# Optimization experiments

Measured on AMD Instinct MI355X. Metric: run time of the kernel, lower is better.

The kernel has to match this reference:

```python
import jax, jax.numpy as jnp
import numpy as np

N = 65536       # num nodes
F = 128         # num_features
D = 256         # embedding_dim
E = N * 8       # num edges
CS = 32         # target_cluster_size
DEPTH = 8
H = 8
NCLS = 10


def setup_inputs() -> dict:
    key = jax.random.key(0)
    ks = jax.random.split(key, 16)
    r = lambda k, shp: (jax.random.normal(k, shp, jnp.float32) * 0.02)
    return {
        "x": jax.random.normal(ks[0], (N, F), jnp.float32),
        "edge_index": jax.random.randint(ks[1], (2, E), 0, N),
        "W_in": r(ks[2], (F, D)), "b_in": jnp.zeros((D,), jnp.float32),
        "W_gat": r(ks[3], (D, D)), "a_src": r(ks[4], (D,)), "a_dst": r(ks[5], (D,)),
        "b_gat": jnp.zeros((D,), jnp.float32),
        "W_emb": r(ks[6], (CS * D, D)), "b_emb": jnp.zeros((D,), jnp.float32),
        "class_tok": r(ks[7], (D,)),
        "ln1_s": jnp.ones((DEPTH, D), jnp.float32), "ln1_b": jnp.zeros((DEPTH, D), jnp.float32),
        "Wqkv": r(ks[8], (DEPTH, D, 3 * D)), "bqkv": jnp.zeros((DEPTH, 3 * D), jnp.float32),
        "Wproj": r(ks[9], (DEPTH, D, D)), "bproj": jnp.zeros((DEPTH, D), jnp.float32),
        "ln2_s": jnp.ones((DEPTH, D), jnp.float32), "ln2_b": jnp.zeros((DEPTH, D), jnp.float32),
        "W1": r(ks[10], (DEPTH, D, 4 * D)), "b1": jnp.zeros((DEPTH, 4 * D), jnp.float32),
        "W2": r(ks[11], (DEPTH, 4 * D, D)), "b2": jnp.zeros((DEPTH, D), jnp.float32),
        "W_cls": r(ks[12], (D, NCLS)), "b_cls": jnp.zeros((NCLS,), jnp.float32),
    }


def _layernorm(x, s, b):
    m = jnp.mean(x, -1, keepdims=True)
    v = jnp.var(x, -1, keepdims=True)
    return (x - m) * jax.lax.rsqrt(v + 1e-5) * s + b


def _forward(x, edge_index, W_in, b_in, W_gat, a_src, a_dst, b_gat, W_emb, b_emb,
             class_tok, ln1_s, ln1_b, Wqkv, bqkv, Wproj, bproj, ln2_s, ln2_b,
             W1, b1, W2, b2, W_cls, b_cls):
    # input_layer: LazyLinear(F -> D)
    h = x @ W_in + b_in                                   # [N, D]
    # GATConv(D -> D), 1 head, add_self_loops=True
    loop = jnp.arange(N)
    src = jnp.concatenate([edge_index[0], loop])          # message source j
    dst = jnp.concatenate([edge_index[1], loop])          # message target i
    Wh = h @ W_gat                                        # [N, D]
    e = jax.nn.leaky_relu((Wh @ a_src)[src] + (Wh @ a_dst)[dst], 0.2)
    emax = jax.ops.segment_max(e, dst, num_segments=N)
    ee = jnp.exp(e - emax[dst])
    denom = jax.ops.segment_sum(ee, dst, num_segments=N)
    alpha = ee / denom[dst]                               # softmax over incoming edges
    h = jax.ops.segment_sum(alpha[:, None] * Wh[src], dst, num_segments=N) + b_gat
    # clusters of 32 contiguous nodes: gather, flatten, embeddings_layer (32*D -> D)
    tok = h.reshape(N // CS, CS * D) @ W_emb + b_emb      # [num_clusters, D]
    seq = jnp.concatenate([class_tok[None, :], tok])[None]  # [1, S, D], S = num_clusters + 1
    scale = (D // H) ** -0.5
    for i in range(DEPTH):
        y = _layernorm(seq, ln1_s[i], ln1_b[i])
        qkv = (y @ Wqkv[i] + bqkv[i]).reshape(1, -1, 3, H, D // H)
        q, k, v = qkv[:, :, 0], qkv[:, :, 1], qkv[:, :, 2]
        att = jax.nn.softmax(jnp.einsum('bshd,bthd->bhst', q, k) * scale, axis=-1)
        o = jnp.einsum('bhst,bthd->bshd', att, v).reshape(1, -1, D)
        seq = seq + (o @ Wproj[i] + bproj[i])
        y = _layernorm(seq, ln2_s[i], ln2_b[i])
        seq = seq + (jax.nn.gelu(y @ W1[i] + b1[i], approximate=False) @ W2[i] + b2[i])
    # to_class on the class token
    return seq[0, 0][None, :] @ W_cls + b_cls             # [1, NCLS]


def reference(x, edge_index, W_in, b_in, W_gat, a_src, a_dst, b_gat, W_emb, b_emb,
              class_tok, ln1_s, ln1_b, Wqkv, bqkv, Wproj, bproj, ln2_s, ln2_b,
              W1, b1, W2, b2, W_cls, b_cls):
    return _forward(x, edge_index, W_in, b_in, W_gat, a_src, a_dst, b_gat, W_emb,
                    b_emb, class_tok, ln1_s, ln1_b, Wqkv, bqkv, Wproj, bproj,
                    ln2_s, ln2_b, W1, b1, W2, b2, W_cls, b_cls)
```

## Files before the change

### kernel.cpp

```cpp
#include <hip/hip_runtime.h>
#include <math.h>

#define N_NODES 65536
#define F_IN 128
#define D_MODEL 256
#define E_EDGES 524288
#define EE_EDGES 589824
#define SEQ_LEN 2049
#define SEQ_PAD 2112
#define NHEAD 8
#define HDIM 32
#define NCLS 10
#define NSPLIT 4

typedef unsigned short u16;
typedef __attribute__((ext_vector_type(8))) short s8v;
typedef __attribute__((ext_vector_type(4))) float f4v;

__device__ __forceinline__ u16 f2bf(float f)
{
    union { float f; unsigned u; } v; v.f = f;
    unsigned r = v.u + 0x7FFF + ((v.u >> 16) & 1);
    return (u16)(r >> 16);
}
__device__ __forceinline__ float bf2f(u16 h)
{
    union { unsigned u; float f; } v; v.u = ((unsigned)h) << 16;
    return v.f;
}

__global__ __launch_bounds__(256) void prep_weight(
    const float* __restrict__ W, u16* __restrict__ Oh, u16* __restrict__ Ol,
    int K, int N, long long strideW, long long strideO, int write_lo)
{
    const float* Wz = W + (size_t)blockIdx.z * strideW;
    u16* Ohz = Oh + (size_t)blockIdx.z * strideO;
    u16* Olz = Ol + (size_t)blockIdx.z * strideO;
    __shared__ u16 th[64][68];
    __shared__ u16 tl[64][68];
    int kb = blockIdx.x * 64, nb = blockIdx.y * 64;
    int t = threadIdx.x;
    int kr = t >> 4, nc = (t & 15) * 4;
#pragma unroll
    for (int i = 0; i < 4; ++i) {
        int k = kr + i * 16;
        float4 v = *(const float4*)(Wz + (size_t)(kb + k) * N + nb + nc);
        float vv[4] = {v.x, v.y, v.z, v.w};
#pragma unroll
        for (int e = 0; e < 4; ++e) {
            u16 h = f2bf(vv[e]);
            th[k][nc + e] = h;
            if (write_lo) tl[k][nc + e] = f2bf(vv[e] - bf2f(h));
        }
    }
    __syncthreads();
    int nr = t >> 4, kc = (t & 15) * 4;
#pragma unroll
    for (int i = 0; i < 4; ++i) {
        int n = nr + i * 16;
        uint2 oh;
        oh.x = (unsigned)th[kc + 0][n] | ((unsigned)th[kc + 1][n] << 16);
        oh.y = (unsigned)th[kc + 2][n] | ((unsigned)th[kc + 3][n] << 16);
        *(uint2*)(Ohz + (size_t)(nb + n) * K + kb + kc) = oh;
        if (write_lo) {
            uint2 ol;
            ol.x = (unsigned)tl[kc + 0][n] | ((unsigned)tl[kc + 1][n] << 16);
            ol.y = (unsigned)tl[kc + 2][n] | ((unsigned)tl[kc + 3][n] << 16);
            *(uint2*)(Olz + (size_t)(nb + n) * K + kb + kc) = ol;
        }
    }
}

template<int ACT, int RES, int ATOM, int OB, int APRE, int TERMS>
__global__ __launch_bounds__(256) void hgemm(
    const void* __restrict__ A, const u16* __restrict__ Al2,
    const u16* __restrict__ Bh, const u16* __restrict__ Bl,
    const float* __restrict__ bias, const float* __restrict__ Rsd,
    float* __restrict__ C, u16* __restrict__ C2,
    int M, int N, int K, int Kc)
{
    __shared__ __align__(16) u16 SS[(TERMS == 3 ? 4 : 2) * 2048];
    u16* const AhS = SS;
    u16* const BhS = SS + 2048;
    u16* const AlS = SS + 4096;
    u16* const BlS = SS + 6144;
    const int tid = threadIdx.x;
    const int bn = blockIdx.x * 64, bm = blockIdx.y * 64;
    const int kb = blockIdx.z * Kc;
    const int r = tid >> 2, cch = tid & 3;
    const int widx = r * 32 + ((cch ^ ((r >> 1) & 3)) << 3);
    const int w = tid >> 6, lane = tid & 63;
    const int wm = w >> 1, wn = w & 1;
    const int lr = lane & 15, lc = lane >> 4;
    const int ar0 = wm * 32 + lr, ar1 = ar0 + 16;
    const int nr0 = wn * 32 + lr, nr1 = nr0 + 16;
    const int ai0 = ar0 * 32 + ((lc ^ ((ar0 >> 1) & 3)) << 3);
    const int ai1 = ar1 * 32 + ((lc ^ ((ar1 >> 1) & 3)) << 3);
    const int bi0 = nr0 * 32 + ((lc ^ ((nr0 >> 1) & 3)) << 3);
    const int bi1 = nr1 * 32 + ((lc ^ ((nr1 >> 1) & 3)) << 3);

    f4v acc00 = {0.f, 0.f, 0.f, 0.f}, acc01 = acc00, acc10 = acc00, acc11 = acc00;

    const int gr = bm + r;
    const float* apf = (const float*)A + (size_t)gr * K + kb + cch * 8;
    const u16*   aph = (const u16*)A + (size_t)gr * K + kb + cch * 8;
    const u16*   apl = Al2 ? Al2 + (size_t)gr * K + kb + cch * 8 : (const u16*)0;
    const u16* bhp = Bh + (size_t)(bn + r) * K + kb + cch * 8;
    const u16* blp = (TERMS == 3) ? Bl + (size_t)(bn + r) * K + kb + cch * 8
                                  : (const u16*)0;

    for (int k0 = 0; k0 < Kc; k0 += 32) {
        s8v hv = {0, 0, 0, 0, 0, 0, 0, 0}, lv = hv;
        if (APRE) {
            if (gr < M) {
                hv = *(const s8v*)aph;
                if (TERMS == 3) lv = *(const s8v*)apl;
            }
        } else {
            float v[8] = {0.f, 0.f, 0.f, 0.f, 0.f, 0.f, 0.f, 0.f};
            if (gr < M) {
                float4 x0 = *(const float4*)apf;
                float4 x1 = *(const float4*)(apf + 4);
                v[0] = x0.x; v[1] = x0.y; v[2] = x0.z; v[3] = x0.w;
                v[4] = x1.x; v[5] = x1.y; v[6] = x1.z; v[7] = x1.w;
            }
#pragma unroll
            for (int e = 0; e < 8; ++e) {
                u16 h = f2bf(v[e]);
                hv[e] = (short)h;
                if (TERMS == 3) lv[e] = (short)f2bf(v[e] - bf2f(h));
            }
        }
        *(s8v*)&AhS[widx] = hv;
        *(s8v*)&BhS[widx] = *(const s8v*)bhp;
        if (TERMS == 3) {
            *(s8v*)&AlS[widx] = lv;
            *(s8v*)&BlS[widx] = *(const s8v*)blp;
        }
        __syncthreads();

        s8v a0h = *(s8v*)&AhS[ai0], a1h = *(s8v*)&AhS[ai1];
        s8v b0h = *(s8v*)&BhS[bi0], b1h = *(s8v*)&BhS[bi1];
        acc00 = __builtin_amdgcn_mfma_f32_16x16x32_bf16(a0h, b0h, acc00, 0, 0, 0);
        acc01 = __builtin_amdgcn_mfma_f32_16x16x32_bf16(a0h, b1h, acc01, 0, 0, 0);
        acc10 = __builtin_amdgcn_mfma_f32_16x16x32_bf16(a1h, b0h, acc10, 0, 0, 0);
        acc11 = __builtin_amdgcn_mfma_f32_16x16x32_bf16(a1h, b1h, acc11, 0, 0, 0);
        if (TERMS == 3) {
            s8v a0l = *(s8v*)&AlS[ai0], a1l = *(s8v*)&AlS[ai1];
            s8v b0l = *(s8v*)&BlS[bi0], b1l = *(s8v*)&BlS[bi1];
            acc00 = __builtin_amdgcn_mfma_f32_16x16x32_bf16(a0h, b0l, acc00, 0, 0, 0);
            acc00 = __builtin_amdgcn_mfma_f32_16x16x32_bf16(a0l, b0h, acc00, 0, 0, 0);
            acc01 = __builtin_amdgcn_mfma_f32_16x16x32_bf16(a0h, b1l, acc01, 0, 0, 0);
            acc01 = __builtin_amdgcn_mfma_f32_16x16x32_bf16(a0l, b1h, acc01, 0, 0, 0);
            acc10 = __builtin_amdgcn_mfma_f32_16x16x32_bf16(a1h, b0l, acc10, 0, 0, 0);
            acc10 = __builtin_amdgcn_mfma_f32_16x16x32_bf16(a1l, b0h, acc10, 0, 0, 0);
            acc11 = __builtin_amdgcn_mfma_f32_16x16x32_bf16(a1h, b1l, acc11, 0, 0, 0);
            acc11 = __builtin_amdgcn_mfma_f32_16x16x32_bf16(a1l, b1h, acc11, 0, 0, 0);
        }
        __syncthreads();
        apf += 32; aph += 32; if (TERMS == 3) apl += 32;
        bhp += 32; if (TERMS == 3) blp += 32;
    }

#pragma unroll
    for (int fg = 0; fg < 4; ++fg) {
        int f = fg >> 1, g = fg & 1;
        f4v a = (fg == 0) ? acc00 : (fg == 1) ? acc01 : (fg == 2) ? acc10 : acc11;
        int col = bn + wn * 32 + g * 16 + lr;
        int row0 = bm + wm * 32 + f * 16 + lc * 4;
#pragma unroll
        for (int j = 0; j < 4; ++j) {
            int rr = row0 + j;
            if (rr < M) {
                float vv = a[j];
                if (ATOM) {
                    atomicAdd(&C[(size_t)rr * N + col], vv);
                } else {
                    if (bias) vv += bias[col];
                    if (ACT == 1) vv = 0.5f * vv * (1.0f + erff(vv * 0.70710678118654752f));
                    if (RES) vv += Rsd[(size_t)rr * N + col];
                    if (OB == 1) ((u16*)C)[(size_t)rr * N + col] = f2bf(vv);
                    else         C[(size_t)rr * N + col] = vv;
                }
            }
        }
    }
    (void)C2;
}

__global__ void init_bias(float* __restrict__ C, const float* __restrict__ bias,
                          int total, int nmask)
{
    int i = blockIdx.x * 256 + threadIdx.x;
    if (i < total) C[i] = bias[i & nmask];
}

__global__ void pad_zero_u32(unsigned* __restrict__ p, int n)
{
    int i = blockIdx.x * 256 + threadIdx.x;
    if (i < n) p[i] = 0u;
}

__global__ void vecmat256(const float* __restrict__ v, const float* __restrict__ W,
                          float* __restrict__ out)
{
    int n = threadIdx.x;
    float acc = 0.f;
    for (int k = 0; k < 256; ++k) acc += v[k] * W[k * 256 + n];
    out[n] = acc;
}

__global__ void gat_init(float* __restrict__ emax, float* __restrict__ denom,
                         int* __restrict__ deg)
{
    int i = blockIdx.x * 256 + threadIdx.x;
    emax[i] = -1e30f;
    denom[i] = 0.f;
    deg[i] = 0;
}

__global__ __launch_bounds__(256) void gat_scores(
    const u16* __restrict__ WH, const float* __restrict__ a_src,
    const float* __restrict__ a_dst, float* __restrict__ s_src,
    float* __restrict__ s_dst)
{
    int gid = blockIdx.x * 256 + threadIdx.x;
    int node = gid >> 6;
    int lane = gid & 63;
    uint2 rv = *(const uint2*)(WH + (size_t)node * D_MODEL + (lane << 2));
    float d0 = __uint_as_float(rv.x << 16);
    float d1 = __uint_as_float(rv.x & 0xffff0000u);
    float d2 = __uint_as_float(rv.y << 16);
    float d3 = __uint_as_float(rv.y & 0xffff0000u);
    float4 asv = *(const float4*)(a_src + (lane << 2));
    float4 adv = *(const float4*)(a_dst + (lane << 2));
    float as = d0 * asv.x + d1 * asv.y + d2 * asv.z + d3 * asv.w;
    float ad = d0 * adv.x + d1 * adv.y + d2 * adv.z + d3 * adv.w;
#pragma unroll
    for (int off = 32; off; off >>= 1) {
        as += __shfl_down(as, off);
        ad += __shfl_down(ad, off);
    }
    if (lane == 0) { s_src[node] = as; s_dst[node] = ad; }
}

__device__ __forceinline__ void atomicMaxFloat(float* addr, float val)
{
    int* ai = (int*)addr;
    int old = __float_as_int(*addr);
    while (__int_as_float(old) < val) {
        int prev = atomicCAS(ai, old, __float_as_int(val));
        if (prev == old) break;
        old = prev;
    }
}

__global__ void edge_pass1(const int* __restrict__ ei, const float* __restrict__ s_src,
                           const float* __restrict__ s_dst, float* __restrict__ e_buf,
                           float* __restrict__ emax, int* __restrict__ deg)
{
    int j = blockIdx.x * 256 + threadIdx.x;
    if (j >= EE_EDGES) return;
    int s, d;
    if (j < E_EDGES) { s = ei[j]; d = ei[E_EDGES + j]; }
    else { s = d = j - E_EDGES; }
    float e = s_src[s] + s_dst[d];
    e = (e > 0.f) ? e : 0.2f * e;
    e_buf[j] = e;
    atomicMaxFloat(&emax[d], e);
    atomicAdd(&deg[d], 1);
}

__global__ void scan1(const int* __restrict__ in, int* __restrict__ out_excl,
                      int* __restrict__ bsum)
{
    __shared__ int s[256];
    int t = threadIdx.x;
    int i = blockIdx.x * 256 + t;
    int v = in[i];
    s[t] = v;
    __syncthreads();
    for (int off = 1; off < 256; off <<= 1) {
        int u = (t >= off) ? s[t - off] : 0;
        __syncthreads();
        s[t] += u;
        __syncthreads();
    }
    out_excl[i] = s[t] - v;
    if (t == 255) bsum[blockIdx.x] = s[255];
}

__global__ void scan2(int* __restrict__ bsum)
{
    __shared__ int s[256];
    int t = threadIdx.x;
    int v = bsum[t];
    s[t] = v;
    __syncthreads();
    for (int off = 1; off < 256; off <<= 1) {
        int u = (t >= off) ? s[t - off] : 0;
        __syncthreads();
        s[t] += u;
        __syncthreads();
    }
    bsum[t] = s[t] - v;
}

__global__ void scan3(int* __restrict__ offs, const int* __restrict__ bsum,
                      int* __restrict__ cur)
{
    int i = blockIdx.x * 256 + threadIdx.x;
    int v = offs[i] + bsum[blockIdx.x];
    offs[i] = v;
    cur[i] = v;
}

__global__ void edge_pass2(const int* __restrict__ ei, const float* __restrict__ e_buf,
                           const float* __restrict__ emax, float* __restrict__ denom,
                           int* __restrict__ cur, int* __restrict__ csr_src,
                           float* __restrict__ csr_w)
{
    int j = blockIdx.x * 256 + threadIdx.x;
    if (j >= EE_EDGES) return;
    int s, d;
    if (j < E_EDGES) { s = ei[j]; d = ei[E_EDGES + j]; }
    else { s = d = j - E_EDGES; }
    float ee = __expf(e_buf[j] - emax[d]);
    atomicAdd(&denom[d], ee);
    int pos = atomicAdd(&cur[d], 1);
    csr_src[pos] = s;
    csr_w[pos] = ee;
}

__global__ __launch_bounds__(256) void gat_aggregate(
    const u16* __restrict__ WH, const int* __restrict__ csr_src,
    const float* __restrict__ csr_w, const int* __restrict__ offs,
    const int* __restrict__ deg, const float* __restrict__ denom,
    const float* __restrict__ b_gat, u16* __restrict__ hH)
{
    int gid = blockIdx.x * 256 + threadIdx.x;
    int node = gid >> 6;
    int lane = gid & 63;
    float inv = 1.0f / denom[node];
    float a0 = 0.f, a1 = 0.f, a2 = 0.f, a3 = 0.f;
    int s0 = offs[node], e0 = s0 + deg[node];
    for (int k = s0; k < e0; ++k) {
        int src = csr_src[k];
        float alpha = csr_w[k] * inv;
        uint2 rv = *(const uint2*)(WH + (size_t)src * D_MODEL + (lane << 2));
        a0 += alpha * __uint_as_float(rv.x << 16);
        a1 += alpha * __uint_as_float(rv.x & 0xffff0000u);
        a2 += alpha * __uint_as_float(rv.y << 16);
        a3 += alpha * __uint_as_float(rv.y & 0xffff0000u);
    }
    float4 bg = *(const float4*)(b_gat + (lane << 2));
    float v0 = a0 + bg.x, v1 = a1 + bg.y, v2 = a2 + bg.z, v3 = a3 + bg.w;
    uint2 ho;
    ho.x = (unsigned)f2bf(v0) | ((unsigned)f2bf(v1) << 16);
    ho.y = (unsigned)f2bf(v2) | ((unsigned)f2bf(v3) << 16);
    *(uint2*)(hH + (size_t)node * D_MODEL + (lane << 2)) = ho;
}

__global__ __launch_bounds__(256) void ln_kernel(
    float* __restrict__ seqio, const float* __restrict__ sc,
    const float* __restrict__ bi, u16* __restrict__ Yh,
    const float* __restrict__ badd)
{
    int row = blockIdx.x;
    int t = threadIdx.x;
    float x = seqio[(size_t)row * 256 + t];
    float sum = x, sq = x * x;
#pragma unroll
    for (int off = 32; off; off >>= 1) {
        sum += __shfl_down(sum, off);
        sq  += __shfl_down(sq, off);
    }
    __shared__ float rs[4], rq[4];
    if ((t & 63) == 0) { rs[t >> 6] = sum; rq[t >> 6] = sq; }
    __syncthreads();
    sum = rs[0] + rs[1] + rs[2] + rs[3];
    sq  = rq[0] + rq[1] + rq[2] + rq[3];
    float mean = sum * (1.f / 256.f);
    float var  = sq * (1.f / 256.f) - mean * mean;
    float r = rsqrtf(var + 1e-5f);
    float y = (x - mean) * r * sc[t] + bi[t];
    Yh[(size_t)row * 256 + t] = f2bf(y);
    seqio[(size_t)row * 256 + t] = x + badd[t];
}

__global__ __launch_bounds__(256) void mfma_attn_split(
    const u16* __restrict__ QKV, float* __restrict__ Opart,
    float* __restrict__ Mpart, float* __restrict__ Lpart)
{
    __shared__ __align__(16) u16 Ks[64 * 32];
    __shared__ __align__(16) u16 Vt[32 * 72];
    __shared__ __align__(16) u16 Ps[4 * 16 * 72];
    const int tid = threadIdx.x;
    const int w = tid >> 6, lane = tid & 63;
    const int g = lane >> 4, ql = lane & 15;
    const int h = blockIdx.y;
    const int sp = blockIdx.z;
    const int t0 = (33 * sp) / NSPLIT, t1 = (33 * (sp + 1)) / NSPLIT;
    const int qbase = blockIdx.x * 64 + w * 16;
    const float scale = 0.17677669529663687f;

    int qrow = qbase + ql; if (qrow > SEQ_LEN - 1) qrow = SEQ_LEN - 1;
    const s8v qfrag = *(const s8v*)(QKV + (size_t)qrow * 768 + h * 32 + g * 8);

    f4v o0 = {0.f, 0.f, 0.f, 0.f}, o1 = o0;
    float m[4], l[4];
#pragma unroll
    for (int r = 0; r < 4; ++r) { m[r] = -1e30f; l[r] = 0.f; }

    const int sr = tid >> 2, sc_ = tid & 3;
    const int kslot = sc_ ^ ((sr >> 1) & 3);
    u16* const psw = &Ps[w * 1152];

    for (int t = t0; t < t1; ++t) {
        __syncthreads();
        {
            int grow = t * 64 + sr;
            const u16* kp = QKV + (size_t)grow * 768 + 256 + h * 32 + sc_ * 8;
            s8v kvv = *(const s8v*)kp;
            s8v vvv = *(const s8v*)(kp + 256);
            *(s8v*)&Ks[sr * 32 + kslot * 8] = kvv;
#pragma unroll
            for (int e = 0; e < 8; ++e) Vt[(sc_ * 8 + e) * 72 + sr] = (u16)vvv[e];
        }
        __syncthreads();

        f4v s[4];
        const f4v zz = {0.f, 0.f, 0.f, 0.f};
#pragma unroll
        for (int c = 0; c < 4; ++c) {
            int kvloc = c * 16 + ql;
            s8v kf = *(s8v*)&Ks[kvloc * 32 + ((g ^ ((kvloc >> 1) & 3)) << 3)];
            s[c] = __builtin_amdgcn_mfma_f32_16x16x32_bf16(qfrag, kf, zz, 0, 0, 0);
            int kvg = t * 64 + kvloc;
            bool valid = (kvg < SEQ_LEN);
#pragma unroll
            for (int r = 0; r < 4; ++r)
                s[c][r] = valid ? s[c][r] * scale : -1e30f;
        }

        float mloc[4];
#pragma unroll
        for (int r = 0; r < 4; ++r) {
            float v = fmaxf(fmaxf(s[0][r], s[1][r]), fmaxf(s[2][r], s[3][r]));
            v = fmaxf(v, __shfl_xor(v, 1));
            v = fmaxf(v, __shfl_xor(v, 2));
            v = fmaxf(v, __shfl_xor(v, 4));
            v = fmaxf(v, __shfl_xor(v, 8));
            mloc[r] = v;
        }
        float fac[4];
#pragma unroll
        for (int r = 0; r < 4; ++r) {
            float mn = fmaxf(m[r], mloc[r]);
            fac[r] = __expf(m[r] - mn);
            m[r] = mn;
        }
#pragma unroll
        for (int c = 0; c < 4; ++c)
#pragma unroll
            for (int r = 0; r < 4; ++r)
                s[c][r] = __expf(s[c][r] - m[r]);
#pragma unroll
        for (int r = 0; r < 4; ++r) {
            float ls = s[0][r] + s[1][r] + s[2][r] + s[3][r];
            ls += __shfl_xor(ls, 1);
            ls += __shfl_xor(ls, 2);
            ls += __shfl_xor(ls, 4);
            ls += __shfl_xor(ls, 8);
            l[r] = l[r] * fac[r] + ls;
            o0[r] *= fac[r];
            o1[r] *= fac[r];
        }

#pragma unroll
        for (int c = 0; c < 4; ++c)
#pragma unroll
            for (int r = 0; r < 4; ++r)
                psw[(g * 4 + r) * 72 + c * 16 + ql] = f2bf(s[c][r]);

#pragma unroll
        for (int kch = 0; kch < 2; ++kch) {
            s8v pf = *(s8v*)&psw[ql * 72 + kch * 32 + g * 8];
            s8v v0 = *(s8v*)&Vt[ql * 72 + kch * 32 + g * 8];
            s8v v1 = *(s8v*)&Vt[(16 + ql) * 72 + kch * 32 + g * 8];
            o0 = __builtin_amdgcn_mfma_f32_16x16x32_bf16(pf, v0, o0, 0, 0, 0);
            o1 = __builtin_amdgcn_mfma_f32_16x16x32_bf16(pf, v1, o1, 0, 0, 0);
        }
    }

#pragma unroll
    for (int r = 0; r < 4; ++r) {
        int q = qbase + g * 4 + r;
        if (q < SEQ_LEN) {
            size_t base = ((size_t)sp * SEQ_PAD + q) * 256 + h * 32;
            Opart[base + ql] = o0[r];
            Opart[base + 16 + ql] = o1[r];
            if (ql == 0) {
                Mpart[((size_t)sp * SEQ_PAD + q) * NHEAD + h] = m[r];
                Lpart[((size_t)sp * SEQ_PAD + q) * NHEAD + h] = l[r];
            }
        }
    }
}

__global__ __launch_bounds__(256) void attn_combine(
    const float* __restrict__ Opart, const float* __restrict__ Mpart,
    const float* __restrict__ Lpart, u16* __restrict__ Oh)
{
    int q = blockIdx.x;
    int t = threadIdx.x;
    int h = t >> 5, d = t & 31;
    float ms[NSPLIT], ls[NSPLIT];
    float M = -1e30f;
#pragma unroll
    for (int s = 0; s < NSPLIT; ++s) {
        ms[s] = Mpart[((size_t)s * SEQ_PAD + q) * NHEAD + h];
        ls[s] = Lpart[((size_t)s * SEQ_PAD + q) * NHEAD + h];
        M = fmaxf(M, ms[s]);
    }
    float L = 0.f, O = 0.f;
#pragma unroll
    for (int s = 0; s < NSPLIT; ++s) {
        float f = __expf(ms[s] - M);
        L += ls[s] * f;
        O += Opart[((size_t)s * SEQ_PAD + q) * 256 + h * 32 + d] * f;
    }
    Oh[(size_t)q * 256 + h * 32 + d] = f2bf(O / L);
}

__global__ void seed_seq(const float* __restrict__ cls, float* __restrict__ seq)
{
    seq[threadIdx.x] = cls[threadIdx.x];
}

__global__ void cls_head(const float* __restrict__ seq, const float* __restrict__ W,
                         const float* __restrict__ b, float* __restrict__ out)
{
    __shared__ float s[256];
    int t = threadIdx.x;
    s[t] = seq[t];
    __syncthreads();
    if (t < NCLS) {
        float acc = b[t];
        for (int k = 0; k < 256; ++k) acc += s[k] * W[k * NCLS + t];
        out[t] = acc;
    }
}

extern "C" void kernel_launch(void* const* d_in, const int* in_sizes, int n_in,
                              void* d_out, int out_size, void* d_ws, size_t ws_size,
                              hipStream_t stream)
{
    (void)in_sizes; (void)n_in; (void)out_size; (void)ws_size;
    const float* x       = (const float*)d_in[0];
    const int*   ei      = (const int*)d_in[1];
    const float* W_in    = (const float*)d_in[2];
    const float* b_in    = (const float*)d_in[3];
    const float* W_gat   = (const float*)d_in[4];
    const float* a_src   = (const float*)d_in[5];
    const float* a_dst   = (const float*)d_in[6];
    const float* b_gat   = (const float*)d_in[7];
    const float* W_emb   = (const float*)d_in[8];
    const float* b_emb   = (const float*)d_in[9];
    const float* cls_tok = (const float*)d_in[10];
    const float* ln1_s   = (const float*)d_in[11];
    const float* ln1_b   = (const float*)d_in[12];
    const float* Wqkv    = (const float*)d_in[13];
    const float* bqkv    = (const float*)d_in[14];
    const float* Wproj   = (const float*)d_in[15];
    const float* bproj   = (const float*)d_in[16];
    const float* ln2_s   = (const float*)d_in[17];
    const float* ln2_b   = (const float*)d_in[18];
    const float* W1      = (const float*)d_in[19];
    const float* b1      = (const float*)d_in[20];
    const float* W2      = (const float*)d_in[21];
    const float* b2      = (const float*)d_in[22];
    const float* W_cls   = (const float*)d_in[23];
    const float* b_cls   = (const float*)d_in[24];
    float* out = (float*)d_out;

    float* ws = (float*)d_ws;
    u16*   bufWHu = (u16*)ws;
    float* seqb  = ws;
    u16*   Yh    = (u16*)(ws + 524544);
    u16*   QKVb  = (u16*)(ws + 1049088);
    u16*   Oh    = (u16*)(ws + 1860096);
    u16*   MLPHh = (u16*)(ws + 2384640);
    u16*   wreg  = (u16*)(ws + 5500000);
    u16* embh  = wreg;
    u16* embl  = wreg + 2097152;
    u16* qkvh  = wreg + 4194304;
    u16* qkvl  = wreg + 5767168;
    u16* projh = wreg + 7340032;
    u16* projl = wreg + 7864320;
    u16* w1h   = wreg + 8388608;
    u16* w1l   = wreg + 10485760;
    u16* w2h   = wreg + 12582912;
    u16* w2l   = wreg + 14680064;
    u16*   hH    = (u16*)(ws + 16777216);
    float* Opart = ws + 16777216;
    float* Mpart = Opart + (size_t)NSPLIT * SEQ_PAD * 256;
    float* Lpart = Mpart + (size_t)NSPLIT * SEQ_PAD * NHEAD;
    float* sm    = ws + 2 * 16777216;
    float* s_src = sm;
    float* s_dst = sm + 65536;
    float* emaxb = sm + 2 * 65536;
    float* denom = sm + 3 * 65536;
    float* e_buf = sm + 4 * 65536;
    float* csr_w = e_buf + 589824;
    float* Wc    = csr_w + 589824;
    float* bc    = Wc + 32768;
    int*   deg     = (int*)(bc + 256);
    int*   offs    = deg + 65536;
    int*   cur     = offs + 65536;
    int*   bsum    = cur + 65536;
    int*   csr_src = bsum + 256;
    u16*   wgTh = (u16*)(csr_src + 589824);
    u16*   wgTl = wgTh + 65536;
    u16*   wcTh = wgTh + 131072;
    u16*   wcTl = wcTh + 32768;

    gat_init<<<256, 256, 0, stream>>>(emaxb, denom, deg);
    prep_weight<<<dim3(4, 4, 1), 256, 0, stream>>>(W_gat, wgTh, wgTl, 256, 256, 0, 0, 1);
    hgemm<0,0,0,0,0,3><<<dim3(4, 2, 1), 256, 0, stream>>>(
        W_in, nullptr, wgTh, wgTl, nullptr, nullptr, Wc, nullptr, 128, 256, 256, 256);
    vecmat256<<<1, 256, 0, stream>>>(b_in, W_gat, bc);
    prep_weight<<<dim3(2, 4, 1), 256, 0, stream>>>(Wc, wcTh, wcTl, 128, 256, 0, 0, 0);
    hgemm<0,0,0,1,0,1><<<dim3(4, 1024, 1), 256, 0, stream>>>(
        x, nullptr, wcTh, nullptr, bc, nullptr, (float*)bufWHu, nullptr,
        N_NODES, 256, 128, 128);
    gat_scores<<<16384, 256, 0, stream>>>(bufWHu, a_src, a_dst, s_src, s_dst);
    edge_pass1<<<EE_EDGES / 256, 256, 0, stream>>>(ei, s_src, s_dst, e_buf, emaxb, deg);
    scan1<<<256, 256, 0, stream>>>(deg, offs, bsum);
    scan2<<<1, 256, 0, stream>>>(bsum);
    scan3<<<256, 256, 0, stream>>>(offs, bsum, cur);
    edge_pass2<<<EE_EDGES / 256, 256, 0, stream>>>(ei, e_buf, emaxb, denom, cur,
                                                   csr_src, csr_w);
    gat_aggregate<<<16384, 256, 0, stream>>>(bufWHu, csr_src, csr_w, offs, deg,
                                             denom, b_gat, hH);

    prep_weight<<<dim3(128, 4, 1), 256, 0, stream>>>(W_emb, embh, embl, 8192, 256, 0, 0, 0);
    prep_weight<<<dim3(4, 12, 8), 256, 0, stream>>>(Wqkv, qkvh, qkvl, 256, 768,
                                                    196608, 196608, 0);
    prep_weight<<<dim3(4, 4, 8), 256, 0, stream>>>(Wproj, projh, projl, 256, 256,
                                                   65536, 65536, 0);
    prep_weight<<<dim3(4, 16, 8), 256, 0, stream>>>(W1, w1h, w1l, 256, 1024,
                                                    262144, 262144, 0);
    prep_weight<<<dim3(16, 4, 8), 256, 0, stream>>>(W2, w2h, w2l, 1024, 256,
                                                    262144, 262144, 0);

    init_bias<<<2048, 256, 0, stream>>>(seqb + 256, b_emb, 2048 * 256, 255);
    hgemm<0,0,1,0,1,1><<<dim3(4, 32, 8), 256, 0, stream>>>(
        (const void*)hH, nullptr, embh, nullptr, nullptr, nullptr, seqb + 256,
        nullptr, 2048, 256, 8192, 1024);
    seed_seq<<<1, 256, 0, stream>>>(cls_tok, seqb);

    pad_zero_u32<<<95, 256, 0, stream>>>(
        (unsigned*)(QKVb + (size_t)SEQ_LEN * 768), (SEQ_PAD - SEQ_LEN) * 768 / 2);

    for (int i = 0; i < 8; ++i) {
        ln_kernel<<<SEQ_LEN, 256, 0, stream>>>(seqb, ln1_s + i * 256,
                                               ln1_b + i * 256, Yh,
                                               bproj + i * 256);
        hgemm<0,0,0,1,1,1><<<dim3(12, 33, 1), 256, 0, stream>>>(
            (const void*)Yh, nullptr, qkvh + (size_t)i * 196608, nullptr,
            bqkv + i * 768, nullptr, (float*)QKVb, nullptr, SEQ_LEN, 768, 256, 256);
        mfma_attn_split<<<dim3(33, NHEAD, NSPLIT), 256, 0, stream>>>(
            QKVb, Opart, Mpart, Lpart);
        attn_combine<<<SEQ_LEN, 256, 0, stream>>>(Opart, Mpart, Lpart, Oh);
        hgemm<0,0,1,0,1,1><<<dim3(4, 33, 4), 256, 0, stream>>>(
            (const void*)Oh, nullptr, projh + (size_t)i * 65536, nullptr,
            nullptr, nullptr, seqb, nullptr, SEQ_LEN, 256, 256, 64);
        ln_kernel<<<SEQ_LEN, 256, 0, stream>>>(seqb, ln2_s + i * 256,
                                               ln2_b + i * 256, Yh,
                                               b2 + i * 256);
        hgemm<1,0,0,1,1,1><<<dim3(16, 33, 1), 256, 0, stream>>>(
            (const void*)Yh, nullptr, w1h + (size_t)i * 262144, nullptr,
            b1 + i * 1024, nullptr, (float*)MLPHh, nullptr, SEQ_LEN, 1024, 256, 256);
        hgemm<0,0,1,0,1,1><<<dim3(4, 33, 4), 256, 0, stream>>>(
            (const void*)MLPHh, nullptr, w2h + (size_t)i * 262144, nullptr,
            nullptr, nullptr, seqb, nullptr, SEQ_LEN, 256, 1024, 256);
    }

    cls_head<<<1, 256, 0, stream>>>(seqb, W_cls, b_cls, out);
}
```

Before: 1.045 ms.

## Fuse LayerNorm into QKV and MLP-up GEMMs by folding scale/bias into weights

Removes the standalone LayerNorm kernels. The LN scale is folded into the bf16 weights at prep time, and the LN bias is folded into the GEMM bias through a new bias_fold kernel. The QKV and W1 GEMMs now read the fp32 residual stream directly and compute per-row mean and rstd in a prologue before normalizing on the fly. Residual biases (bproj, b2) move into the split-K atomic GEMMs on z==0, and the seq init is merged into one kernel. This cuts launches and the Yh round trip, but each GEMM block re-reads its A rows to compute the statistics, and the variance is computed as E[x^2]-mu^2.

```diff
diff --git a/kernel.cpp b/kernel.cpp
--- a/kernel.cpp
+++ b/kernel.cpp
@@ -31,11 +31,13 @@
 
 __global__ __launch_bounds__(256) void prep_weight(
     const float* __restrict__ W, u16* __restrict__ Oh, u16* __restrict__ Ol,
-    int K, int N, long long strideW, long long strideO, int write_lo)
+    int K, int N, long long strideW, long long strideO, int write_lo,
+    const float* __restrict__ scale)
 {
     const float* Wz = W + (size_t)blockIdx.z * strideW;
     u16* Ohz = Oh + (size_t)blockIdx.z * strideO;
     u16* Olz = Ol + (size_t)blockIdx.z * strideO;
+    const float* scz = scale ? scale + (size_t)blockIdx.z * D_MODEL : nullptr;
     __shared__ u16 th[64][68];
     __shared__ u16 tl[64][68];
     int kb = blockIdx.x * 64, nb = blockIdx.y * 64;
@@ -44,8 +46,9 @@
 #pragma unroll
     for (int i = 0; i < 4; ++i) {
         int k = kr + i * 16;
+        float sv = scz ? scz[kb + k] : 1.f;
         float4 v = *(const float4*)(Wz + (size_t)(kb + k) * N + nb + nc);
-        float vv[4] = {v.x, v.y, v.z, v.w};
+        float vv[4] = {v.x * sv, v.y * sv, v.z * sv, v.w * sv};
 #pragma unroll
         for (int e = 0; e < 4; ++e) {
             u16 h = f2bf(vv[e]);
@@ -71,7 +74,21 @@
     }
 }
 
-template<int ACT, int RES, int ATOM, int OB, int APRE, int TERMS>
+__global__ void bias_fold(const float* __restrict__ lnb, const float* __restrict__ W,
+                          const float* __restrict__ b0, float* __restrict__ out,
+                          int N, long long strideW)
+{
+    int z = blockIdx.y;
+    int n = blockIdx.x * 256 + threadIdx.x;
+    if (n >= N) return;
+    const float* Wz = W + (size_t)z * strideW;
+    const float* lz = lnb + (size_t)z * D_MODEL;
+    float acc = b0[(size_t)z * N + n];
+    for (int k = 0; k < D_MODEL; ++k) acc += lz[k] * Wz[(size_t)k * N + n];
+    out[(size_t)z * N + n] = acc;
+}
+
+template<int ACT, int RES, int ATOM, int OB, int APRE, int TERMS, int LNA>
 __global__ __launch_bounds__(256) void hgemm(
     const void* __restrict__ A, const u16* __restrict__ Al2,
     const u16* __restrict__ Bh, const u16* __restrict__ Bl,
@@ -109,6 +126,28 @@
     const u16* blp = (TERMS == 3) ? Bl + (size_t)(bn + r) * K + kb + cch * 8
                                   : (const u16*)0;
 
+    float mu_r = 0.f, rs_r = 1.f;
+    if (LNA) {
+        float s1 = 0.f, s2 = 0.f;
+        if (gr < M) {
+            const float* rowp = apf;
+            for (int ks = 0; ks < Kc / 32; ++ks) {
+                float4 a0 = *(const float4*)(rowp);
+                float4 a1 = *(const float4*)(rowp + 4);
+                s1 += a0.x + a0.y + a0.z + a0.w + a1.x + a1.y + a1.z + a1.w;
+                s2 += a0.x*a0.x + a0.y*a0.y + a0.z*a0.z + a0.w*a0.w
+                    + a1.x*a1.x + a1.y*a1.y + a1.z*a1.z + a1.w*a1.w;
+                rowp += 32;
+            }
+        }
+        s1 += __shfl_xor(s1, 1); s1 += __shfl_xor(s1, 2);
+        s2 += __shfl_xor(s2, 1); s2 += __shfl_xor(s2, 2);
+        float mu = s1 * (1.f / 256.f);
+        float var = s2 * (1.f / 256.f) - mu * mu;
+        mu_r = mu;
+        rs_r = rsqrtf(var + 1e-5f);
+    }
+
     for (int k0 = 0; k0 < Kc; k0 += 32) {
         s8v hv = {0, 0, 0, 0, 0, 0, 0, 0}, lv = hv;
         if (APRE) {
@@ -126,9 +165,10 @@
             }
 #pragma unroll
             for (int e = 0; e < 8; ++e) {
-                u16 h = f2bf(v[e]);
+                float vv = LNA ? (v[e] - mu_r) * rs_r : v[e];
+                u16 h = f2bf(vv);
                 hv[e] = (short)h;
-                if (TERMS == 3) lv[e] = (short)f2bf(v[e] - bf2f(h));
+                if (TERMS == 3) lv[e] = (short)f2bf(vv - bf2f(h));
             }
         }
         *(s8v*)&AhS[widx] = hv;
@@ -174,6 +214,7 @@
             if (rr < M) {
                 float vv = a[j];
                 if (ATOM) {
+                    if (bias && blockIdx.z == 0) vv += bias[col];
                     atomicAdd(&C[(size_t)rr * N + col], vv);
                 } else {
                     if (bias) vv += bias[col];
@@ -188,11 +229,12 @@
     (void)C2;
 }
 
-__global__ void init_bias(float* __restrict__ C, const float* __restrict__ bias,
-                          int total, int nmask)
-{
-    int i = blockIdx.x * 256 + threadIdx.x;
-    if (i < total) C[i] = bias[i & nmask];
+__global__ void init_seq(float* __restrict__ seq, const float* __restrict__ bias,
+                         const float* __restrict__ cls)
+{
+    int row = blockIdx.x;
+    int t = threadIdx.x;
+    seq[(size_t)row * 256 + t] = (row == 0) ? cls[t] : bias[t];
 }
 
 __global__ void pad_zero_u32(unsigned* __restrict__ p, int n)
@@ -361,33 +403,6 @@
     *(uint2*)(hH + (size_t)node * D_MODEL + (lane << 2)) = ho;
 }
 
-__global__ __launch_bounds__(256) void ln_kernel(
-    float* __restrict__ seqio, const float* __restrict__ sc,
-    const float* __restrict__ bi, u16* __restrict__ Yh,
-    const float* __restrict__ badd)
-{
-    int row = blockIdx.x;
-    int t = threadIdx.x;
-    float x = seqio[(size_t)row * 256 + t];
-    float sum = x, sq = x * x;
-#pragma unroll
-    for (int off = 32; off; off >>= 1) {
-        sum += __shfl_down(sum, off);
-        sq  += __shfl_down(sq, off);
-    }
-    __shared__ float rs[4], rq[4];
-    if ((t & 63) == 0) { rs[t >> 6] = sum; rq[t >> 6] = sq; }
-    __syncthreads();
-    sum = rs[0] + rs[1] + rs[2] + rs[3];
-    sq  = rq[0] + rq[1] + rq[2] + rq[3];
-    float mean = sum * (1.f / 256.f);
-    float var  = sq * (1.f / 256.f) - mean * mean;
-    float r = rsqrtf(var + 1e-5f);
-    float y = (x - mean) * r * sc[t] + bi[t];
-    Yh[(size_t)row * 256 + t] = f2bf(y);
-    seqio[(size_t)row * 256 + t] = x + badd[t];
-}
-
 __global__ __launch_bounds__(256) void mfma_attn_split(
     const u16* __restrict__ QKV, float* __restrict__ Opart,
     float* __restrict__ Mpart, float* __restrict__ Lpart)
@@ -531,11 +546,6 @@
         O += Opart[((size_t)s * SEQ_PAD + q) * 256 + h * 32 + d] * f;
     }
     Oh[(size_t)q * 256 + h * 32 + d] = f2bf(O / L);
-}
-
-__global__ void seed_seq(const float* __restrict__ cls, float* __restrict__ seq)
-{
-    seq[threadIdx.x] = cls[threadIdx.x];
 }
 
 __global__ void cls_head(const float* __restrict__ seq, const float* __restrict__ W,
@@ -587,10 +597,11 @@
     float* ws = (float*)d_ws;
     u16*   bufWHu = (u16*)ws;
     float* seqb  = ws;
-    u16*   Yh    = (u16*)(ws + 524544);
     u16*   QKVb  = (u16*)(ws + 1049088);
     u16*   Oh    = (u16*)(ws + 1860096);
     u16*   MLPHh = (u16*)(ws + 2384640);
+    float* qkvBias = ws + 3500000;
+    float* w1Bias  = qkvBias + 8 * 768;
     u16*   wreg  = (u16*)(ws + 5500000);
     u16* embh  = wreg;
     u16* embl  = wreg + 2097152;
@@ -626,12 +637,14 @@
     u16*   wcTl = wcTh + 32768;
 
     gat_init<<<256, 256, 0, stream>>>(emaxb, denom, deg);
-    prep_weight<<<dim3(4, 4, 1), 256, 0, stream>>>(W_gat, wgTh, wgTl, 256, 256, 0, 0, 1);
-    hgemm<0,0,0,0,0,3><<<dim3(4, 2, 1), 256, 0, stream>>>(
+    prep_weight<<<dim3(4, 4, 1), 256, 0, stream>>>(W_gat, wgTh, wgTl, 256, 256,
+                                                   0, 0, 1, nullptr);
+    hgemm<0,0,0,0,0,3,0><<<dim3(4, 2, 1), 256, 0, stream>>>(
         W_in, nullptr, wgTh, wgTl, nullptr, nullptr, Wc, nullptr, 128, 256, 256, 256);
     vecmat256<<<1, 256, 0, stream>>>(b_in, W_gat, bc);
-    prep_weight<<<dim3(2, 4, 1), 256, 0, stream>>>(Wc, wcTh, wcTl, 128, 256, 0, 0, 0);
-    hgemm<0,0,0,1,0,1><<<dim3(4, 1024, 1), 256, 0, stream>>>(
+    prep_weight<<<dim3(2, 4, 1), 256, 0, stream>>>(Wc, wcTh, wcTl, 128, 256,
+                                                   0, 0, 0, nullptr);
+    hgemm<0,0,0,1,0,1,0><<<dim3(4, 1024, 1), 256, 0, stream>>>(
         x, nullptr, wcTh, nullptr, bc, nullptr, (float*)bufWHu, nullptr,
         N_NODES, 256, 128, 128);
     gat_scores<<<16384, 256, 0, stream>>>(bufWHu, a_src, a_dst, s_src, s_dst);
@@ -644,47 +657,45 @@
     gat_aggregate<<<16384, 256, 0, stream>>>(bufWHu, csr_src, csr_w, offs, deg,
                                              denom, b_gat, hH);
 
-    prep_weight<<<dim3(128, 4, 1), 256, 0, stream>>>(W_emb, embh, embl, 8192, 256, 0, 0, 0);
+    prep_weight<<<dim3(128, 4, 1), 256, 0, stream>>>(W_emb, embh, embl, 8192, 256,
+                                                     0, 0, 0, nullptr);
     prep_weight<<<dim3(4, 12, 8), 256, 0, stream>>>(Wqkv, qkvh, qkvl, 256, 768,
-                                                    196608, 196608, 0);
+                                                    196608, 196608, 0, ln1_s);
     prep_weight<<<dim3(4, 4, 8), 256, 0, stream>>>(Wproj, projh, projl, 256, 256,
-                                                   65536, 65536, 0);
+                                                   65536, 65536, 0, nullptr);
     prep_weight<<<dim3(4, 16, 8), 256, 0, stream>>>(W1, w1h, w1l, 256, 1024,
-                                                    262144, 262144, 0);
+                                                    262144, 262144, 0, ln2_s);
     prep_weight<<<dim3(16, 4, 8), 256, 0, stream>>>(W2, w2h, w2l, 1024, 256,
-                                                    262144, 262144, 0);
-
-    init_bias<<<2048, 256, 0, stream>>>(seqb + 256, b_emb, 2048 * 256, 255);
-    hgemm<0,0,1,0,1,1><<<dim3(4, 32, 8), 256, 0, stream>>>(
+                                                    262144, 262144, 0, nullptr);
+    bias_fold<<<dim3(3, 8), 256, 0, stream>>>(ln1_b, Wqkv, bqkv, qkvBias, 768, 196608);
+    bias_fold<<<dim3(4, 8), 256, 0, stream>>>(ln2_b, W1, b1, w1Bias, 1024, 262144);
+
+    init_seq<<<SEQ_LEN, 256, 0, stream>>>(seqb, b_emb, cls_tok);
+    hgemm<0,0,1,0,1,1,0><<<dim3(4, 32, 8), 256, 0, stream>>>(
         (const void*)hH, nullptr, embh, nullptr, nullptr, nullptr, seqb + 256,
         nullptr, 2048, 256, 8192, 1024);
-    seed_seq<<<1, 256, 0, stream>>>(cls_tok, seqb);
 
     pad_zero_u32<<<95, 256, 0, stream>>>(
         (unsigned*)(QKVb + (size_t)SEQ_LEN * 768), (SEQ_PAD - SEQ_LEN) * 768 / 2);
 
     for (int i = 0; i < 8; ++i) {
-        ln_kernel<<<SEQ_LEN, 256, 0, stream>>>(seqb, ln1_s + i * 256,
-                                               ln1_b + i * 256, Yh,
-                                               bproj + i * 256);
-        hgemm<0,0,0,1,1,1><<<dim3(12, 33, 1), 256, 0, stream>>>(
-            (const void*)Yh, nullptr, qkvh + (size_t)i * 196608, nullptr,
-            bqkv + i * 768, nullptr, (float*)QKVb, nullptr, SEQ_LEN, 768, 256, 256);
+        hgemm<0,0,0,1,0,1,1><<<dim3(12, 33, 1), 256, 0, stream>>>(
+            (const void*)seqb, nullptr, qkvh + (size_t)i * 196608, nullptr,
+            qkvBias + (size_t)i * 768, nullptr, (float*)QKVb, nullptr,
+            SEQ_LEN, 768, 256, 256);
         mfma_attn_split<<<dim3(33, NHEAD, NSPLIT), 256, 0, stream>>>(
             QKVb, Opart, Mpart, Lpart);
         attn_combine<<<SEQ_LEN, 256, 0, stream>>>(Opart, Mpart, Lpart, Oh);
-        hgemm<0,0,1,0,1,1><<<dim3(4, 33, 4), 256, 0, stream>>>(
+        hgemm<0,0,1,0,1,1,0><<<dim3(4, 33, 4), 256, 0, stream>>>(
             (const void*)Oh, nullptr, projh + (size_t)i * 65536, nullptr,
-            nullptr, nullptr, seqb, nullptr, SEQ_LEN, 256, 256, 64);
-        ln_kernel<<<SEQ_LEN, 256, 0, stream>>>(seqb, ln2_s + i * 256,
-                                               ln2_b + i * 256, Yh,
-                                               b2 + i * 256);
-        hgemm<1,0,0,1,1,1><<<dim3(16, 33, 1), 256, 0, stream>>>(
-            (const void*)Yh, nullptr, w1h + (size_t)i * 262144, nullptr,
-            b1 + i * 1024, nullptr, (float*)MLPHh, nullptr, SEQ_LEN, 1024, 256, 256);
-        hgemm<0,0,1,0,1,1><<<dim3(4, 33, 4), 256, 0, stream>>>(
+            bproj + (size_t)i * 256, nullptr, seqb, nullptr, SEQ_LEN, 256, 256, 64);
+        hgemm<1,0,0,1,0,1,1><<<dim3(16, 33, 1), 256, 0, stream>>>(
+            (const void*)seqb, nullptr, w1h + (size_t)i * 262144, nullptr,
+            w1Bias + (size_t)i * 1024, nullptr, (float*)MLPHh, nullptr,
+            SEQ_LEN, 1024, 256, 256);
+        hgemm<0,0,1,0,1,1,0><<<dim3(4, 33, 4), 256, 0, stream>>>(
             (const void*)MLPHh, nullptr, w2h + (size_t)i * 262144, nullptr,
-            nullptr, nullptr, seqb, nullptr, SEQ_LEN, 256, 1024, 256);
+            b2 + (size_t)i * 256, nullptr, seqb, nullptr, SEQ_LEN, 256, 1024, 256);
     }
 
     cls_head<<<1, 256, 0, stream>>>(seqb, W_cls, b_cls, out);
```

New measurement: 1.133 ms. +8.4%, slower.
